# Kernel optimization log

Hardware: AMD Instinct MI355X
Metric: run time of the kernel (lower is better)

Reference implementation:

```python
import jax, jax.numpy as jnp
import numpy as np

N = 100000
E = 600000
D_IN = 128
D_OUT = 128


def setup_inputs() -> dict:
    key = jax.random.key(0)
    k1, k2, k3, k4 = jax.random.split(key, 4)
    H = jax.random.normal(k1, (N, D_IN), dtype=jnp.float32)
    edge_index = jax.random.randint(k2, (2, E), 0, N, dtype=jnp.int64)
    # torch Linear default init: U(-1/sqrt(in), 1/sqrt(in)); scale-equivalent randn ok for reference
    bound = 1.0 / np.sqrt(D_IN)
    W = jax.random.uniform(k3, (D_OUT, D_IN), minval=-bound, maxval=bound, dtype=jnp.float32)
    b = jax.random.uniform(k4, (D_OUT,), minval=-bound, maxval=bound, dtype=jnp.float32)
    return {"H": H, "edge_index": edge_index, "W": W, "b": b}


def reference(H, edge_index, W, b):
    n = H.shape[0]
    # add self loops (PyG add_self_loops appends [i, i] for every node)
    loops = jnp.arange(n, dtype=edge_index.dtype)
    row = jnp.concatenate([edge_index[0], loops])  # [E + N]
    col = jnp.concatenate([edge_index[1], loops])
    # degree of destination nodes (row), as in pyg.utils.degree(row, N)
    deg = jax.ops.segment_sum(jnp.ones_like(row, dtype=H.dtype), row, num_segments=n)
    deg_inv_sqrt = jnp.where(deg > 0, jax.lax.rsqrt(jnp.maximum(deg, 1.0)), 0.0)
    norm = deg_inv_sqrt[row] * deg_inv_sqrt[col]  # [E + N]
    # linear transform on nodes
    Hl = H @ W.T + b  # [N, D_OUT]
    # gather source features, scale, scatter-add to destinations
    msg = Hl[col] * norm[:, None]  # [E + N, D_OUT]
    out = jax.ops.segment_sum(msg, row, num_segments=n)
    return jax.nn.relu(out)
```

## Files before the change

### kernel.cpp

```cpp
#include <hip/hip_runtime.h>
#include <hip/hip_bf16.h>

#define N_NODES 100000
#define N_EDGES 600000
#define DIM 128
#define CAP 40

typedef __attribute__((ext_vector_type(8))) short short8;
typedef __attribute__((ext_vector_type(4))) float f32x4;

static __device__ __forceinline__ short f2bf(float f) {
    return __builtin_bit_cast(short, __float2bfloat16(f));
}
static __device__ __forceinline__ unsigned pack2(float a, float b) {
    unsigned lo = (unsigned short)__builtin_bit_cast(short, __float2bfloat16(a));
    unsigned hi = (unsigned short)__builtin_bit_cast(short, __float2bfloat16(b));
    return lo | (hi << 16);
}

__global__ __launch_bounds__(256) void iota_kernel(int* __restrict__ cursor) {
    int i = blockIdx.x * 256 + threadIdx.x;
    if (i < N_NODES) cursor[i] = i * CAP;
}

__global__ __launch_bounds__(256) void fill_kernel(
    const int* __restrict__ erow, const int* __restrict__ ecol,
    int* __restrict__ cursor, int* __restrict__ bucket)
{
    int e = blockIdx.x * 256 + threadIdx.x;
    if (e < N_EDGES) {
        int r = erow[e];
        if ((unsigned)r < (unsigned)N_NODES) {
            int pos = atomicAdd(&cursor[r], 1);
            if ((unsigned)pos < (unsigned)(N_NODES * CAP)) bucket[pos] = ecol[e];
        }
    }
}

__global__ __launch_bounds__(256) void linear_mfma(
    const float* __restrict__ H, const float* __restrict__ W,
    const float* __restrict__ b, const int* __restrict__ cursor,
    __hip_bfloat16* __restrict__ Hl)
{
    __shared__ __hip_bfloat16 Wb[DIM][DIM + 8];

    const int t = threadIdx.x;
    for (int i = t; i < DIM * (DIM / 4); i += 256) {
        int row = i >> 5, c4 = i & 31;
        float4 w4 = ((const float4*)W)[i];
        __hip_bfloat16* dst = &Wb[row][c4 * 4];
        dst[0] = __float2bfloat16(w4.x);
        dst[1] = __float2bfloat16(w4.y);
        dst[2] = __float2bfloat16(w4.z);
        dst[3] = __float2bfloat16(w4.w);
    }
    __syncthreads();

    const int wave = t >> 6;
    const int lane = t & 63;
    const int quad = lane >> 4;
    const int l16  = lane & 15;
    const int node = blockIdx.x * 64 + wave * 16 + l16;
    const bool valid = node < N_NODES;

    float4 h[4][2];
    float dn = 0.f;
    if (valid) {
        const float4* hp = (const float4*)(H + (size_t)node * DIM);
        #pragma unroll
        for (int ks = 0; ks < 4; ++ks) {
            h[ks][0] = hp[ks * 8 + quad * 2];
            h[ks][1] = hp[ks * 8 + quad * 2 + 1];
        }
        int d = cursor[node] - node * CAP;
        d = min(max(d, 0), CAP);
        dn = rsqrtf((float)d + 1.0f);
    } else {
        #pragma unroll
        for (int ks = 0; ks < 4; ++ks)
            h[ks][0] = h[ks][1] = make_float4(0.f, 0.f, 0.f, 0.f);
    }

    f32x4 acc[8];
    #pragma unroll
    for (int mt = 0; mt < 8; ++mt) acc[mt] = (f32x4){0.f, 0.f, 0.f, 0.f};

    #pragma unroll
    for (int ks = 0; ks < 4; ++ks) {
        const int k0 = ks * 32 + quad * 8;
        short8 hfr;
        hfr[0] = f2bf(h[ks][0].x); hfr[1] = f2bf(h[ks][0].y);
        hfr[2] = f2bf(h[ks][0].z); hfr[3] = f2bf(h[ks][0].w);
        hfr[4] = f2bf(h[ks][1].x); hfr[5] = f2bf(h[ks][1].y);
        hfr[6] = f2bf(h[ks][1].z); hfr[7] = f2bf(h[ks][1].w);

        #pragma unroll
        for (int mt = 0; mt < 8; ++mt) {
            short8 wfr = *(const short8*)&Wb[mt * 16 + l16][k0];
            acc[mt] = __builtin_amdgcn_mfma_f32_16x16x32_bf16(wfr, hfr, acc[mt], 0, 0, 0);
        }
    }

    if (valid) {
        #pragma unroll
        for (int mt = 0; mt < 8; ++mt) {
            float4 b4 = *(const float4*)(b + mt * 16 + quad * 4);
            uint2 pk;
            pk.x = pack2((acc[mt][0] + b4.x) * dn, (acc[mt][1] + b4.y) * dn);
            pk.y = pack2((acc[mt][2] + b4.z) * dn, (acc[mt][3] + b4.w) * dn);
            *(uint2*)(Hl + (size_t)node * DIM + mt * 16 + quad * 4) = pk;
        }
    }
}

__global__ __launch_bounds__(256) void gather_kernel(
    const int* __restrict__ cursor, const int* __restrict__ bucket,
    const __hip_bfloat162* __restrict__ Hl2, float* __restrict__ out)
{
    int node = blockIdx.x * 4 + (threadIdx.x >> 6);
    if (node >= N_NODES) return;
    int lane = threadIdx.x & 63;

    int d = cursor[node] - node * CAP;
    d = min(max(d, 0), CAP);
    float dn = rsqrtf((float)d + 1.0f);

    __hip_bfloat162 hs = Hl2[(size_t)node * (DIM / 2) + lane];
    float2 acc;
    acc.x = __low2float(hs);
    acc.y = __high2float(hs);

    const int4* bp = (const int4*)(bucket + (size_t)node * CAP);
    for (int j = 0; j < d; j += 8) {
        int4 ia = bp[(j >> 2)];
        int4 ib = bp[(j >> 2) + 1];
        int ids[8] = {ia.x, ia.y, ia.z, ia.w, ib.x, ib.y, ib.z, ib.w};
        __hip_bfloat162 rows[8];
        float wgt[8];
        #pragma unroll
        for (int k = 0; k < 8; ++k) {
            bool v = (j + k) < d;
            int idx = v ? ids[k] : 0;
            idx = ((unsigned)idx < (unsigned)N_NODES) ? idx : 0;
            wgt[k] = v ? 1.0f : 0.0f;
            rows[k] = Hl2[(size_t)idx * (DIM / 2) + lane];
        }
        #pragma unroll
        for (int k = 0; k < 8; ++k) {
            acc.x = fmaf(__low2float(rows[k]),  wgt[k], acc.x);
            acc.y = fmaf(__high2float(rows[k]), wgt[k], acc.y);
        }
    }

    acc.x = fmaxf(acc.x * dn, 0.f);
    acc.y = fmaxf(acc.y * dn, 0.f);
    ((float2*)out)[(size_t)node * (DIM / 2) + lane] = acc;
}

extern "C" void kernel_launch(void* const* d_in, const int* in_sizes, int n_in,
                              void* d_out, int out_size, void* d_ws, size_t ws_size,
                              hipStream_t stream) {
    const float* H  = (const float*)d_in[0];
    const int*   ei = (const int*)d_in[1];
    const float* W  = (const float*)d_in[2];
    const float* b  = (const float*)d_in[3];
    float* out = (float*)d_out;

    char* ws = (char*)d_ws;
    __hip_bfloat16* Hl = (__hip_bfloat16*)(ws);
    int* cursor = (int*)(ws + 25600000);
    int* bucket = (int*)(ws + 26000000);

    const int* erow = ei;
    const int* ecol = ei + N_EDGES;

    iota_kernel<<<(N_NODES + 255) / 256, 256, 0, stream>>>(cursor);
    fill_kernel<<<(N_EDGES + 255) / 256, 256, 0, stream>>>(erow, ecol, cursor, bucket);
    linear_mfma<<<(N_NODES + 63) / 64, 256, 0, stream>>>(H, W, b, cursor, Hl);
    gather_kernel<<<(N_NODES + 3) / 4, 256, 0, stream>>>(cursor, bucket,
                                                         (const __hip_bfloat162*)Hl, out);
}
```

Baseline: 183.6 us.

## Gather neighbor rows with 16-byte loads across four lane groups per wave

The gather kernel now splits each wave into four 16-lane groups. Each group fetches a different neighbor's full bf16 row with 16-byte loads, where before every lane made a 4-byte load per neighbor. Neighbor ids are loaded once per node and distributed by shuffles, and partial sums are combined with xor shuffles before the ReLU store. The linear kernel also grows to 512-thread blocks covering 128 nodes each. The aim is fewer, wider memory transactions per edge, at the cost of cross-lane reductions and idle lanes when the degree is not a multiple of four.

```diff
diff --git a/kernel.cpp b/kernel.cpp
--- a/kernel.cpp
+++ b/kernel.cpp
@@ -16,6 +16,12 @@
     unsigned lo = (unsigned short)__builtin_bit_cast(short, __float2bfloat16(a));
     unsigned hi = (unsigned short)__builtin_bit_cast(short, __float2bfloat16(b));
     return lo | (hi << 16);
+}
+static __device__ __forceinline__ float bflo(unsigned u) {
+    return __builtin_bit_cast(float, u << 16);
+}
+static __device__ __forceinline__ float bfhi(unsigned u) {
+    return __builtin_bit_cast(float, u & 0xffff0000u);
 }
 
 __global__ __launch_bounds__(256) void iota_kernel(int* __restrict__ cursor) {
@@ -37,7 +43,7 @@
     }
 }
 
-__global__ __launch_bounds__(256) void linear_mfma(
+__global__ __launch_bounds__(512) void linear_mfma(
     const float* __restrict__ H, const float* __restrict__ W,
     const float* __restrict__ b, const int* __restrict__ cursor,
     __hip_bfloat16* __restrict__ Hl)
@@ -45,7 +51,7 @@
     __shared__ __hip_bfloat16 Wb[DIM][DIM + 8];
 
     const int t = threadIdx.x;
-    for (int i = t; i < DIM * (DIM / 4); i += 256) {
+    for (int i = t; i < DIM * (DIM / 4); i += 512) {
         int row = i >> 5, c4 = i & 31;
         float4 w4 = ((const float4*)W)[i];
         __hip_bfloat16* dst = &Wb[row][c4 * 4];
@@ -60,7 +66,7 @@
     const int lane = t & 63;
     const int quad = lane >> 4;
     const int l16  = lane & 15;
-    const int node = blockIdx.x * 64 + wave * 16 + l16;
+    const int node = blockIdx.x * 128 + wave * 16 + l16;
     const bool valid = node < N_NODES;
 
     float4 h[4][2];
@@ -115,46 +121,64 @@
 
 __global__ __launch_bounds__(256) void gather_kernel(
     const int* __restrict__ cursor, const int* __restrict__ bucket,
-    const __hip_bfloat162* __restrict__ Hl2, float* __restrict__ out)
+    const __hip_bfloat16* __restrict__ Hl, float* __restrict__ out)
 {
     int node = blockIdx.x * 4 + (threadIdx.x >> 6);
     if (node >= N_NODES) return;
-    int lane = threadIdx.x & 63;
+    const int lane = threadIdx.x & 63;
+    const int g  = lane >> 4;
+    const int gl = lane & 15;
+
+    uint4 selfv = make_uint4(0u, 0u, 0u, 0u);
+    if (g == 0) selfv = *(const uint4*)(Hl + (size_t)node * DIM + gl * 8);
 
     int d = cursor[node] - node * CAP;
     d = min(max(d, 0), CAP);
     float dn = rsqrtf((float)d + 1.0f);
 
-    __hip_bfloat162 hs = Hl2[(size_t)node * (DIM / 2) + lane];
-    float2 acc;
-    acc.x = __low2float(hs);
-    acc.y = __high2float(hs);
-
-    const int4* bp = (const int4*)(bucket + (size_t)node * CAP);
-    for (int j = 0; j < d; j += 8) {
-        int4 ia = bp[(j >> 2)];
-        int4 ib = bp[(j >> 2) + 1];
-        int ids[8] = {ia.x, ia.y, ia.z, ia.w, ib.x, ib.y, ib.z, ib.w};
-        __hip_bfloat162 rows[8];
-        float wgt[8];
-        #pragma unroll
-        for (int k = 0; k < 8; ++k) {
-            bool v = (j + k) < d;
-            int idx = v ? ids[k] : 0;
-            idx = ((unsigned)idx < (unsigned)N_NODES) ? idx : 0;
-            wgt[k] = v ? 1.0f : 0.0f;
-            rows[k] = Hl2[(size_t)idx * (DIM / 2) + lane];
-        }
-        #pragma unroll
-        for (int k = 0; k < 8; ++k) {
-            acc.x = fmaf(__low2float(rows[k]),  wgt[k], acc.x);
-            acc.y = fmaf(__high2float(rows[k]), wgt[k], acc.y);
-        }
-    }
-
-    acc.x = fmaxf(acc.x * dn, 0.f);
-    acc.y = fmaxf(acc.y * dn, 0.f);
-    ((float2*)out)[(size_t)node * (DIM / 2) + lane] = acc;
+    int id_all = -1;
+    if (lane < CAP) {
+        int v = bucket[(size_t)node * CAP + lane];
+        id_all = (lane < d && (unsigned)v < (unsigned)N_NODES) ? v : -1;
+    }
+
+    float acc[8] = {0.f, 0.f, 0.f, 0.f, 0.f, 0.f, 0.f, 0.f};
+
+    for (int j = 0; j < d; j += 4) {
+        int id = __shfl(id_all, j + g, 64);
+        float wgt = (id >= 0) ? 1.0f : 0.0f;
+        int idx = (id >= 0) ? id : 0;
+        uint4 rv = *(const uint4*)(Hl + (size_t)idx * DIM + gl * 8);
+        unsigned rw[4] = {rv.x, rv.y, rv.z, rv.w};
+        #pragma unroll
+        for (int hh = 0; hh < 4; ++hh) {
+            acc[2 * hh + 0] = fmaf(bflo(rw[hh]), wgt, acc[2 * hh + 0]);
+            acc[2 * hh + 1] = fmaf(bfhi(rw[hh]), wgt, acc[2 * hh + 1]);
+        }
+    }
+
+    {
+        unsigned sw[4] = {selfv.x, selfv.y, selfv.z, selfv.w};
+        #pragma unroll
+        for (int hh = 0; hh < 4; ++hh) {
+            acc[2 * hh + 0] += bflo(sw[hh]);
+            acc[2 * hh + 1] += bfhi(sw[hh]);
+        }
+    }
+
+    #pragma unroll
+    for (int k = 0; k < 8; ++k) {
+        acc[k] += __shfl_xor(acc[k], 16, 64);
+        acc[k] += __shfl_xor(acc[k], 32, 64);
+        acc[k] = fmaxf(acc[k] * dn, 0.f);
+    }
+
+    if (g < 2) {
+        float4 v;
+        if (g == 0) v = make_float4(acc[0], acc[1], acc[2], acc[3]);
+        else        v = make_float4(acc[4], acc[5], acc[6], acc[7]);
+        *(float4*)(out + (size_t)node * DIM + gl * 8 + g * 4) = v;
+    }
 }
 
 extern "C" void kernel_launch(void* const* d_in, const int* in_sizes, int n_in,
@@ -176,7 +200,6 @@
 
     iota_kernel<<<(N_NODES + 255) / 256, 256, 0, stream>>>(cursor);
     fill_kernel<<<(N_EDGES + 255) / 256, 256, 0, stream>>>(erow, ecol, cursor, bucket);
-    linear_mfma<<<(N_NODES + 63) / 64, 256, 0, stream>>>(H, W, b, cursor, Hl);
-    gather_kernel<<<(N_NODES + 3) / 4, 256, 0, stream>>>(cursor, bucket,
-                                                         (const __hip_bfloat162*)Hl, out);
-}
+    linear_mfma<<<(N_NODES + 127) / 128, 512, 0, stream>>>(H, W, b, cursor, Hl);
+    gather_kernel<<<(N_NODES + 3) / 4, 256, 0, stream>>>(cursor, bucket, Hl, out);
+}
```

After: 188.0 us. 2.4% more time.
